# Kernel tuning notes

Hardware: AMD Instinct MI355X
Metric: run time of the kernel (lower is better)

## Reference

```python
import jax, jax.numpy as jnp
import numpy as np

FS = 4096.0
TRAIN_KERNEL = 4
TRAIN_STRIDE = 0.25
BATCH = 1024
NPERSEG = 4096          # fftlength * fs
NOVERLAP = NPERSEG // 2 # default overlap
FL, FH = 20.0, 500.0


def _welch(data):
    """Faithful port of _torch_welch with average='mean' (which is a SUM over segments
    in the original code), off by the same constant factor as the original."""
    N, nsample = data.shape
    nstride = NPERSEG - NOVERLAP
    nseg = int(np.ceil((nsample - NPERSEG) / nstride)) + 1
    # frame indices [nseg, nperseg] (static numpy -> cheap gather)
    idx = np.arange(nseg)[:, None] * nstride + np.arange(NPERSEG)[None, :]
    frames = data[:, idx]                                   # [N, nseg, nperseg]
    n = np.arange(NPERSEG)
    window = (0.5 - 0.5 * np.cos(2.0 * np.pi * n / NPERSEG)).astype(np.float32) * 2.0  # periodic hann * 2
    fd = jnp.fft.rfft(frames * window, axis=-1)             # [N, nseg, nfreq]
    power = jnp.real(fd) ** 2 + jnp.imag(fd) ** 2
    psd = jnp.sum(power, axis=1)                            # original 'mean' branch uses sum
    T = nsample * FS
    return psd / T                                          # [N, nfreq]


def setup_inputs() -> dict:
    key = jax.random.key(0)
    k1, k2 = jax.random.split(key)
    T = int(TRAIN_KERNEL * FS)  # 16384
    pred = jax.random.normal(k1, (BATCH, T), dtype=jnp.float32)
    target = jax.random.normal(k2, (BATCH, T), dtype=jnp.float32)
    return {"pred": pred, "target": target}


def reference(pred, target):
    res = target - pred
    s = int(TRAIN_STRIDE * FS)                     # 1024 samples per stride
    shape_x = int(TRAIN_KERNEL / TRAIN_STRIDE)     # 16
    # cross[i] = res[:, i*s:(i+1)*s].flatten() -> reshape/transpose, no loop
    def to_cross(x):
        return x[:, : shape_x * s].reshape(BATCH, shape_x, s).transpose(1, 0, 2).reshape(shape_x, BATCH * s)
    cross_res = to_cross(res)
    cross_target = to_cross(target)

    psd_res = _welch(cross_res)                    # [shape_x, nfreq]
    psd_target = _welch(cross_target)

    nfreq = NPERSEG // 2 + 1
    freq = np.linspace(0.0, FS / 2.0, nfreq)
    mask = jnp.asarray((FL < freq) & (freq < FH))
    dfreq = float(freq[1] - freq[0])
    scale = FH - FL

    psd_res = jnp.where(mask, psd_res, 0.0)
    psd_ratio = psd_res / psd_target
    loss = jnp.sum(psd_ratio, axis=1) * dfreq / scale  # [shape_x]
    return jnp.mean(loss[-8:]) * loss.shape[0]
```

## Files before the change

kernel.cpp:

```cpp
#include <hip/hip_runtime.h>

#define NSEG 511
#define NROWS 8
#define ROW0 8
#define K0 21
#define KEND 500
#define NFREQ 479
#define ACC_STRIDE 512
#define ACC_ELEMS (2 * NROWS * ACC_STRIDE)
#define NREP 8
#define SPB 8
#define NGROUPS 64
#define NBLOCKS (2 * NROWS * NGROUPS)

__device__ __forceinline__ int sw(int i) { return i ^ (((i >> 5) & 7) << 2); }
__device__ __forceinline__ int revq(int m) { return 64 * (m & 7) + 8 * ((m >> 3) & 7) + (m >> 6); }

__device__ __forceinline__ float2 cmul(float2 a, float2 b) {
    return make_float2(fmaf(a.x, b.x, -a.y * b.y), fmaf(a.x, b.y, a.y * b.x));
}
__device__ __forceinline__ float2 cadd(float2 a, float2 b) { return make_float2(a.x + b.x, a.y + b.y); }
__device__ __forceinline__ float2 csub(float2 a, float2 b) { return make_float2(a.x - b.x, a.y - b.y); }

__device__ __forceinline__ void dft8(float2& x0, float2& x1, float2& x2, float2& x3,
                                     float2& x4, float2& x5, float2& x6, float2& x7) {
    const float C45 = 0.70710678118654752440f;
    float2 t0 = cadd(x0, x4), u0 = csub(x0, x4);
    float2 t1 = cadd(x1, x5), u1 = csub(x1, x5);
    float2 t2 = cadd(x2, x6), u2 = csub(x2, x6);
    float2 t3 = cadd(x3, x7), u3 = csub(x3, x7);
    float2 s0 = cadd(t0, t2), d0 = csub(t0, t2);
    float2 s1 = cadd(t1, t3), d1 = csub(t1, t3);
    float2 v1 = make_float2(C45 * (u1.x + u1.y), C45 * (u1.y - u1.x));
    float2 v2 = make_float2(u2.y, -u2.x);
    float2 v3 = make_float2(C45 * (u3.y - u3.x), -C45 * (u3.x + u3.y));
    float2 s2 = cadd(u0, v2), d2 = csub(u0, v2);
    float2 s3 = cadd(v1, v3), d3 = csub(v1, v3);
    float2 mid1 = make_float2(d1.y, -d1.x);
    float2 mid3 = make_float2(d3.y, -d3.x);
    x0 = cadd(s0, s1); x4 = csub(s0, s1);
    x2 = cadd(d0, mid1); x6 = csub(d0, mid1);
    x1 = cadd(s2, s3); x5 = csub(s2, s3);
    x3 = cadd(d2, mid3); x7 = csub(d2, mid3);
}

__device__ __forceinline__ void twiddle8cs(float2& x1, float2& x2, float2& x3, float2& x4,
                                           float2& x5, float2& x6, float2& x7,
                                           float c, float s) {
    float2 w1 = make_float2(c, s);
    float2 w2 = cmul(w1, w1);
    float2 w3 = cmul(w2, w1);
    float2 w4 = cmul(w2, w2);
    float2 w5 = cmul(w4, w1);
    float2 w6 = cmul(w3, w3);
    float2 w7 = cmul(w4, w3);
    x1 = cmul(x1, w1); x2 = cmul(x2, w2); x3 = cmul(x3, w3);
    x4 = cmul(x4, w4); x5 = cmul(x5, w5); x6 = cmul(x6, w6);
    x7 = cmul(x7, w7);
}

__global__ __launch_bounds__(256)
void psd_kernel(const float* __restrict__ pred,
                const float* __restrict__ target,
                float* __restrict__ acc) {
    __shared__ float2 buf[2048];

    const int bid = blockIdx.x;
    const int grp = bid % NGROUPS;
    const int row = (bid / NGROUPS) % NROWS + ROW0;
    const int sig = bid / (NGROUPS * NROWS);
    const int tid = threadIdx.x;
    const int seg0 = grp * SPB;
    const int ns = (seg0 + SPB <= NSEG) ? SPB : (NSEG - seg0);

    const float2* t2p = (const float2*)target;
    const float2* p2p = (const float2*)pred;

    const int base = 2 * seg0 * 8192 + row * 512 + tid;
#define LOADRAW(X, IDX)                                                      \
    {                                                                        \
        int _i = (IDX);                                                      \
        float2 v = t2p[_i];                                                  \
        if (sig == 0) { float2 p = p2p[_i]; v.x -= p.x; v.y -= p.y; }        \
        X = v;                                                               \
    }
    float2 r0, r1, r2, r3, r4, r5, r6, r7;
    LOADRAW(r0, base)
    LOADRAW(r1, base + 256)
    LOADRAW(r2, base + 8192)
    LOADRAW(r3, base + 8448)
    LOADRAW(r4, base + 16384)
    LOADRAW(r5, base + 16640)
    LOADRAW(r6, base + 24576)
    LOADRAW(r7, base + 24832)

    const float WA = 3.06796157577128245e-3f;
    const float H  = 0.70710678118654752440f;
    float sa, ca;
    __sincosf((float)tid * WA, &sa, &ca);
    float sb, cb;
    __sincosf((float)(tid & 31) * -2.45436926061702596e-2f, &sb, &cb);
    float cc, ss;
    {
        const float TC1 = 0.98078528040323044913f, TS1 = -0.19509032201612826785f;
        const float TC2 = 0.92387953251128675613f, TS2 = -0.38268343236508977173f;
        const float TC3 = 0.83146961230254523708f, TS3 = -0.55557023301960222474f;
        int mq = tid & 3;
        cc = (mq & 2) ? ((mq & 1) ? TC3 : TC2) : ((mq & 1) ? TC1 : 1.0f);
        ss = (mq & 2) ? ((mq & 1) ? TS3 : TS2) : ((mq & 1) ? TS1 : 0.0f);
    }

    const int sigma = (tid & 0xC0) | ((tid & 7) << 3) | ((tid >> 3) & 7);
    const int k1 = K0 + sigma;
    const bool has2 = (sigma < KEND - K0 - 256);

    float sn0, cs0;
    __sincosf(-1.53398078788564123e-3f * (float)k1, &sn0, &cs0);

    const int qA1 = sw(4 * revq(k1)) >> 1;
    const int qB1 = sw(4 * revq(512 - k1)) >> 1;

    float pw1 = 0.0f, pw2 = 0.0f;
    float4* b4 = (float4*)buf;

    #pragma unroll 1
    for (int s = 0; s < ns; ++s) {
        const float CD = 0.99999882344642529f;
        const float SD = 1.53398018628476550e-3f;
        float cat = ca, sat = sa;
        asm volatile("" : "+v"(cat), "+v"(sat));
        float2 wv0, wv1, wv2, wv3, wv4, wv5, wv6, wv7;
#define MKW(W, CE, SE) { float cr = (CE), sr = (SE);                         \
        W = make_float2(1.0f - cr, 1.0f - (cr * CD - sr * SD)); }
        MKW(wv0, cat, sat)
        MKW(wv1, H * (cat - sat), H * (sat + cat))
        MKW(wv2, -sat, cat)
        MKW(wv3, -H * (cat + sat), H * (cat - sat))
        MKW(wv4, -cat, -sat)
        MKW(wv5, H * (sat - cat), -H * (sat + cat))
        MKW(wv6, sat, -cat)
        MKW(wv7, H * (cat + sat), H * (sat - cat))
#undef MKW

        float2 x0 = make_float2(r0.x * wv0.x, r0.y * wv0.y);
        float2 x1 = make_float2(r1.x * wv1.x, r1.y * wv1.y);
        float2 x2 = make_float2(r2.x * wv2.x, r2.y * wv2.y);
        float2 x3 = make_float2(r3.x * wv3.x, r3.y * wv3.y);
        float2 x4 = make_float2(r4.x * wv4.x, r4.y * wv4.y);
        float2 x5 = make_float2(r5.x * wv5.x, r5.y * wv5.y);
        float2 x6 = make_float2(r6.x * wv6.x, r6.y * wv6.y);
        float2 x7 = make_float2(r7.x * wv7.x, r7.y * wv7.y);

        if (s + 1 < ns) {
            r0 = r4; r1 = r5; r2 = r6; r3 = r7;
            int nb = base + (s + 1) * 16384;
            LOADRAW(r4, nb + 16384)
            LOADRAW(r5, nb + 16640)
            LOADRAW(r6, nb + 24576)
            LOADRAW(r7, nb + 24832)
        }

        dft8(x0, x1, x2, x3, x4, x5, x6, x7);
        twiddle8cs(x1, x2, x3, x4, x5, x6, x7, ca, -sa);
        buf[sw(tid)]        = x0;
        buf[sw(tid + 256)]  = x1;
        buf[sw(tid + 512)]  = x2;
        buf[sw(tid + 768)]  = x3;
        buf[sw(tid + 1024)] = x4;
        buf[sw(tid + 1280)] = x5;
        buf[sw(tid + 1536)] = x6;
        buf[sw(tid + 1792)] = x7;
        __syncthreads();

        {
            const int baseB = (tid & 31) + 256 * (tid >> 5);
            x0 = buf[sw(baseB)];
            x1 = buf[sw(baseB + 32)];
            x2 = buf[sw(baseB + 64)];
            x3 = buf[sw(baseB + 96)];
            x4 = buf[sw(baseB + 128)];
            x5 = buf[sw(baseB + 160)];
            x6 = buf[sw(baseB + 192)];
            x7 = buf[sw(baseB + 224)];
            dft8(x0, x1, x2, x3, x4, x5, x6, x7);
            twiddle8cs(x1, x2, x3, x4, x5, x6, x7, cb, sb);
            buf[sw(baseB)]       = x0;
            buf[sw(baseB + 32)]  = x1;
            buf[sw(baseB + 64)]  = x2;
            buf[sw(baseB + 96)]  = x3;
            buf[sw(baseB + 128)] = x4;
            buf[sw(baseB + 160)] = x5;
            buf[sw(baseB + 192)] = x6;
            buf[sw(baseB + 224)] = x7;
        }

        {
            const int baseC = (tid & 3) + 32 * ((tid >> 2) & 7) + 256 * (tid >> 5);
            x0 = buf[sw(baseC)];
            x1 = buf[sw(baseC + 4)];
            x2 = buf[sw(baseC + 8)];
            x3 = buf[sw(baseC + 12)];
            x4 = buf[sw(baseC + 16)];
            x5 = buf[sw(baseC + 20)];
            x6 = buf[sw(baseC + 24)];
            x7 = buf[sw(baseC + 28)];
            dft8(x0, x1, x2, x3, x4, x5, x6, x7);
            twiddle8cs(x1, x2, x3, x4, x5, x6, x7, cc, ss);
            buf[sw(baseC)]      = x0;
            buf[sw(baseC + 4)]  = x1;
            buf[sw(baseC + 8)]  = x2;
            buf[sw(baseC + 12)] = x3;
            buf[sw(baseC + 16)] = x4;
            buf[sw(baseC + 20)] = x5;
            buf[sw(baseC + 24)] = x6;
            buf[sw(baseC + 28)] = x7;
        }
        __syncthreads();

        {
            float4 lo = b4[qA1], hi = b4[qA1 + 1];
            float2 zk = make_float2((lo.x + hi.x) + (lo.z + hi.z),
                                    (lo.y + hi.y) + (lo.w + hi.w));
            lo = b4[qB1]; hi = b4[qB1 + 1];
            float D0x = lo.x - hi.x, D0y = lo.y - hi.y;
            float D1x = lo.z - hi.z, D1y = lo.w - hi.w;
            float2 zn = make_float2(D0x - D1y, D0y + D1x);
            float Ex = 0.5f * (zk.x + zn.x);
            float Ey = 0.5f * (zk.y - zn.y);
            float Ox = 0.5f * (zk.y + zn.y);
            float Oy = -0.5f * (zk.x - zn.x);
            float xr = Ex + Ox * cs0 - Oy * sn0;
            float xi = Ey + Ox * sn0 + Oy * cs0;
            pw1 += xr * xr + xi * xi;
        }
        if (has2) {
            float c0 = cs0, s0 = sn0;
            asm volatile("" : "+v"(c0), "+v"(s0));
            const float CU = 0.98078528040323044913f;
            const float SU = 0.19509032201612826785f;
            float cs1 = c0 * CU + s0 * SU;
            float sn1 = s0 * CU - c0 * SU;
            float4 lo = b4[qA1 + 8], hi = b4[qA1 + 9];
            float2 zk = make_float2((lo.x + hi.x) + (lo.z + hi.z),
                                    (lo.y + hi.y) + (lo.w + hi.w));
            lo = b4[qB1 - 8]; hi = b4[qB1 - 7];
            float D0x = lo.x - hi.x, D0y = lo.y - hi.y;
            float D1x = lo.z - hi.z, D1y = lo.w - hi.w;
            float2 zn = make_float2(D0x - D1y, D0y + D1x);
            float Ex = 0.5f * (zk.x + zn.x);
            float Ey = 0.5f * (zk.y - zn.y);
            float Ox = 0.5f * (zk.y + zn.y);
            float Oy = -0.5f * (zk.x - zn.x);
            float xr = Ex + Ox * cs1 - Oy * sn1;
            float xi = Ey + Ox * sn1 + Oy * cs1;
            pw2 += xr * xr + xi * xi;
        }
        if (s + 1 < ns) __syncthreads();
    }

    {
        float* accR = acc + (bid & (NREP - 1)) * ACC_ELEMS;
        int i0 = (sig * NROWS + (row - ROW0)) * ACC_STRIDE;
        atomicAdd(&accR[i0 + sigma], pw1);
        if (has2) atomicAdd(&accR[i0 + 256 + sigma], pw2);
    }
#undef LOADRAW
}

__global__ __launch_bounds__(256)
void reduce_kernel(const float* __restrict__ acc, float* __restrict__ out) {
    __shared__ float sh[256];
    int tid = threadIdx.x;
    float sum = 0.0f;
    for (int n = tid; n < NROWS * NFREQ; n += 256) {
        int r = n / NFREQ, k = n % NFREQ;
        float num = 0.0f, den = 0.0f;
        #pragma unroll
        for (int rep = 0; rep < NREP; ++rep) {
            num += acc[rep * ACC_ELEMS + r * ACC_STRIDE + k];
            den += acc[rep * ACC_ELEMS + (NROWS + r) * ACC_STRIDE + k];
        }
        sum += num / den;
    }
    sh[tid] = sum;
    __syncthreads();
    for (int s = 128; s > 0; s >>= 1) {
        if (tid < s) sh[tid] += sh[tid + s];
        __syncthreads();
    }
    if (tid == 0) out[0] = sh[0] * (1.0f / 240.0f);
}

extern "C" void kernel_launch(void* const* d_in, const int* in_sizes, int n_in,
                              void* d_out, int out_size, void* d_ws, size_t ws_size,
                              hipStream_t stream) {
    const float* pred = (const float*)d_in[0];
    const float* target = (const float*)d_in[1];
    float* acc = (float*)d_ws;

    hipMemsetAsync(acc, 0, NREP * ACC_ELEMS * sizeof(float), stream);
    psd_kernel<<<NBLOCKS, 256, 0, stream>>>(pred, target, acc);
    reduce_kernel<<<1, 256, 0, stream>>>(acc, (float*)d_out);
}
```

Before: 169.0 us.

## Write last FFT stage to separate natural-order LDS buffer and drop trailing barrier

The final radix stage now writes its outputs into a second shared-memory array laid out in natural frequency order, with padding, instead of back into the swizzled buffer. Each thread handles a contiguous bin and reads four float2 values instead of two float4 pairs. Because the extraction reads a separate array, the end-of-iteration barrier is removed so the next segment's stores can overlap the reads. The cost is extra LDS per block, which may lower occupancy, and the next iteration's final write to the natural-order array must still be guarded by the in-loop barriers.

```diff
diff --git a/kernel.cpp b/kernel.cpp
--- a/kernel.cpp
+++ b/kernel.cpp
@@ -14,7 +14,7 @@
 #define NBLOCKS (2 * NROWS * NGROUPS)
 
 __device__ __forceinline__ int sw(int i) { return i ^ (((i >> 5) & 7) << 2); }
-__device__ __forceinline__ int revq(int m) { return 64 * (m & 7) + 8 * ((m >> 3) & 7) + (m >> 6); }
+__device__ __forceinline__ int natq(int m) { return m + 4 * ((m >> 4) & 3); }
 
 __device__ __forceinline__ float2 cmul(float2 a, float2 b) {
     return make_float2(fmaf(a.x, b.x, -a.y * b.y), fmaf(a.x, b.y, a.y * b.x));
@@ -64,6 +64,7 @@
                 const float* __restrict__ target,
                 float* __restrict__ acc) {
     __shared__ float2 buf[2048];
+    __shared__ float2 nat[2064];
 
     const int bid = blockIdx.x;
     const int grp = bid % NGROUPS;
@@ -110,18 +111,19 @@
         ss = (mq & 2) ? ((mq & 1) ? TS3 : TS2) : ((mq & 1) ? TS1 : 0.0f);
     }
 
-    const int sigma = (tid & 0xC0) | ((tid & 7) << 3) | ((tid >> 3) & 7);
-    const int k1 = K0 + sigma;
-    const bool has2 = (sigma < KEND - K0 - 256);
+    const int k1 = K0 + tid;
+    const bool has2 = (tid < KEND - K0 - 256);
 
     float sn0, cs0;
     __sincosf(-1.53398078788564123e-3f * (float)k1, &sn0, &cs0);
 
-    const int qA1 = sw(4 * revq(k1)) >> 1;
-    const int qB1 = sw(4 * revq(512 - k1)) >> 1;
+    const int qk = natq(k1);
+    const int qn = natq(512 - k1);
+
+    const int mb = 8 * ((tid >> 2) & 7) + (tid >> 5);
+    const int natC = natq(mb) + 513 * (tid & 3);
 
     float pw1 = 0.0f, pw2 = 0.0f;
-    float4* b4 = (float4*)buf;
 
     #pragma unroll 1
     for (int s = 0; s < ns; ++s) {
@@ -206,24 +208,26 @@
             x7 = buf[sw(baseC + 28)];
             dft8(x0, x1, x2, x3, x4, x5, x6, x7);
             twiddle8cs(x1, x2, x3, x4, x5, x6, x7, cc, ss);
-            buf[sw(baseC)]      = x0;
-            buf[sw(baseC + 4)]  = x1;
-            buf[sw(baseC + 8)]  = x2;
-            buf[sw(baseC + 12)] = x3;
-            buf[sw(baseC + 16)] = x4;
-            buf[sw(baseC + 20)] = x5;
-            buf[sw(baseC + 24)] = x6;
-            buf[sw(baseC + 28)] = x7;
+            nat[natC]       = x0;
+            nat[natC + 64]  = x1;
+            nat[natC + 128] = x2;
+            nat[natC + 192] = x3;
+            nat[natC + 256] = x4;
+            nat[natC + 320] = x5;
+            nat[natC + 384] = x6;
+            nat[natC + 448] = x7;
         }
         __syncthreads();
 
         {
-            float4 lo = b4[qA1], hi = b4[qA1 + 1];
-            float2 zk = make_float2((lo.x + hi.x) + (lo.z + hi.z),
-                                    (lo.y + hi.y) + (lo.w + hi.w));
-            lo = b4[qB1]; hi = b4[qB1 + 1];
-            float D0x = lo.x - hi.x, D0y = lo.y - hi.y;
-            float D1x = lo.z - hi.z, D1y = lo.w - hi.w;
+            float2 a0 = nat[qk],        a1 = nat[qk + 513];
+            float2 a2 = nat[qk + 1026], a3 = nat[qk + 1539];
+            float2 zk = make_float2((a0.x + a1.x) + (a2.x + a3.x),
+                                    (a0.y + a1.y) + (a2.y + a3.y));
+            float2 b0 = nat[qn],        b1 = nat[qn + 513];
+            float2 b2 = nat[qn + 1026], b3 = nat[qn + 1539];
+            float D0x = b0.x - b2.x, D0y = b0.y - b2.y;
+            float D1x = b1.x - b3.x, D1y = b1.y - b3.y;
             float2 zn = make_float2(D0x - D1y, D0y + D1x);
             float Ex = 0.5f * (zk.x + zn.x);
             float Ey = 0.5f * (zk.y - zn.y);
@@ -240,12 +244,14 @@
             const float SU = 0.19509032201612826785f;
             float cs1 = c0 * CU + s0 * SU;
             float sn1 = s0 * CU - c0 * SU;
-            float4 lo = b4[qA1 + 8], hi = b4[qA1 + 9];
-            float2 zk = make_float2((lo.x + hi.x) + (lo.z + hi.z),
-                                    (lo.y + hi.y) + (lo.w + hi.w));
-            lo = b4[qB1 - 8]; hi = b4[qB1 - 7];
-            float D0x = lo.x - hi.x, D0y = lo.y - hi.y;
-            float D1x = lo.z - hi.z, D1y = lo.w - hi.w;
+            float2 a0 = nat[qk + 256],  a1 = nat[qk + 769];
+            float2 a2 = nat[qk + 1282], a3 = nat[qk + 1795];
+            float2 zk = make_float2((a0.x + a1.x) + (a2.x + a3.x),
+                                    (a0.y + a1.y) + (a2.y + a3.y));
+            float2 b0 = nat[qn - 256],  b1 = nat[qn + 257];
+            float2 b2 = nat[qn + 770],  b3 = nat[qn + 1283];
+            float D0x = b0.x - b2.x, D0y = b0.y - b2.y;
+            float D1x = b1.x - b3.x, D1y = b1.y - b3.y;
             float2 zn = make_float2(D0x - D1y, D0y + D1x);
             float Ex = 0.5f * (zk.x + zn.x);
             float Ey = 0.5f * (zk.y - zn.y);
@@ -255,14 +261,13 @@
             float xi = Ey + Ox * sn1 + Oy * cs1;
             pw2 += xr * xr + xi * xi;
         }
-        if (s + 1 < ns) __syncthreads();
     }
 
     {
         float* accR = acc + (bid & (NREP - 1)) * ACC_ELEMS;
         int i0 = (sig * NROWS + (row - ROW0)) * ACC_STRIDE;
-        atomicAdd(&accR[i0 + sigma], pw1);
-        if (has2) atomicAdd(&accR[i0 + 256 + sigma], pw2);
+        atomicAdd(&accR[i0 + tid], pw1);
+        if (has2) atomicAdd(&accR[i0 + 256 + tid], pw2);
     }
 #undef LOADRAW
 }
```

Result: faster. 163.5 us (-3.3%).
